# Performance work log

Hardware: AMD Instinct MI355X
Metric: run time of the kernel (lower is better)

Reference implementation:

```python
import jax, jax.numpy as jnp
import numpy as np

B, S, D, H, G = 4, 2048, 1024, 16, 32
HD = D // H
LN_EPS = 1e-5


def _lin_init(key, fan_in, fan_out):
    kw, kb = jax.random.split(key)
    bound = 1.0 / np.sqrt(fan_in)
    W = jax.random.uniform(kw, (fan_in, fan_out), jnp.float32, -bound, bound)
    b = jax.random.uniform(kb, (fan_out,), jnp.float32, -bound, bound)
    return W, b


def setup_inputs() -> dict:
    key = jax.random.key(0)
    ks = jax.random.split(key, 9)
    x = jax.random.normal(ks[0], (B, S, D), jnp.float32)
    geo_features = jax.random.normal(ks[1], (B, G), jnp.float32)
    Wq, bq = _lin_init(ks[2], D, D)
    Wk, bk = _lin_init(ks[3], D, D)
    Wv, bv = _lin_init(ks[4], D, D)
    Wo, bo = _lin_init(ks[5], D, D)
    ge_W1, ge_b1 = _lin_init(ks[6], G, D)
    ln_g = jnp.ones((D,), jnp.float32)
    ln_b = jnp.zeros((D,), jnp.float32)
    ge_W2, ge_b2 = _lin_init(ks[7], D, D)
    gm_W, gm_b = _lin_init(ks[8], D, H)
    return dict(x=x, geo_features=geo_features, Wq=Wq, bq=bq, Wk=Wk, bk=bk,
                Wv=Wv, bv=bv, Wo=Wo, bo=bo, ge_W1=ge_W1, ge_b1=ge_b1,
                ln_g=ln_g, ln_b=ln_b, ge_W2=ge_W2, ge_b2=ge_b2,
                gm_W=gm_W, gm_b=gm_b)


def reference(x, geo_features, Wq, bq, Wk, bk, Wv, bv, Wo, bo,
              ge_W1, ge_b1, ln_g, ln_b, ge_W2, ge_b2, gm_W, gm_b):
    # QKV projections -> (B, H, S, HD)
    def split_heads(t):
        return t.reshape(B, S, H, HD).transpose(0, 2, 1, 3)
    Q = split_heads(x @ Wq + bq)
    K = split_heads(x @ Wk + bk)
    V = split_heads(x @ Wv + bv)

    # geo encoder: Linear -> LayerNorm -> ReLU -> Linear
    h = geo_features @ ge_W1 + ge_b1                      # (B, D)
    mu = jnp.mean(h, axis=-1, keepdims=True)
    var = jnp.mean(jnp.square(h - mu), axis=-1, keepdims=True)
    h = (h - mu) / jnp.sqrt(var + LN_EPS) * ln_g + ln_b
    h = jax.nn.relu(h)
    geo_encoded = h @ ge_W2 + ge_b2                       # (B, D)
    geo_mod = jax.nn.sigmoid(geo_encoded @ gm_W + gm_b)   # (B, H)

    scale = 1.0 / np.sqrt(HD)
    scores = jnp.einsum('bhqd,bhkd->bhqk', Q, K) * scale  # (B, H, S, S)
    scores = scores * (1.0 + geo_mod[:, :, None, None])
    attn = jax.nn.softmax(scores, axis=-1)                # dropout in eval mode: identity
    ctx = jnp.einsum('bhqk,bhkd->bhqd', attn, V)          # (B, H, S, HD)
    ctx = ctx.transpose(0, 2, 1, 3).reshape(B, S, D)
    out = ctx @ Wo + bo
    return out, attn
```

## Files before the change

### kernel.cpp

```cpp
#include <hip/hip_runtime.h>

typedef __attribute__((ext_vector_type(8))) short bf16x8;
typedef __attribute__((ext_vector_type(4))) float f32x4;
typedef __attribute__((ext_vector_type(4))) unsigned short us4;
typedef unsigned short u16;

#define MB (1024*1024)

#define WAITV(N) asm volatile("s_waitcnt vmcnt(" #N ")" ::: "memory")
#define WAITL0() asm volatile("s_waitcnt lgkmcnt(0)" ::: "memory")
#define BAR()    __builtin_amdgcn_s_barrier()
#define SCHEDB() __builtin_amdgcn_sched_barrier(0)

__device__ __forceinline__ u16 f2bf(float f) {
    unsigned u = __float_as_uint(f);
    unsigned r = (u + 0x7fffu + ((u >> 16) & 1u)) >> 16;
    return (u16)r;
}

__device__ __forceinline__ unsigned cvtpk(float a, float b) {
    unsigned r;
    asm("v_cvt_pk_bf16_f32 %0, %1, %2" : "=v"(r) : "v"(a), "v"(b));
    return r;
}

__device__ __forceinline__ f32x4 mfma16(bf16x8 a, bf16x8 b, f32x4 c) {
    return __builtin_amdgcn_mfma_f32_16x16x32_bf16(a, b, c, 0, 0, 0);
}

__device__ __forceinline__ void gload16(const void* g, void* l) {
    __builtin_amdgcn_global_load_lds(
        (__attribute__((address_space(1))) void*)(unsigned long long)g,
        (__attribute__((address_space(3))) void*)l, 16, 0, 0);
}

__global__ __launch_bounds__(256) void k_cvtx(const float* __restrict__ x, u16* __restrict__ xb) {
    const long long i = (long long)blockIdx.x * 256 + threadIdx.x;
    const float4* xp = (const float4*)x;
    float4 a = xp[i*2], b = xp[i*2+1];
    bf16x8 o;
    o[0]=(short)f2bf(a.x); o[1]=(short)f2bf(a.y); o[2]=(short)f2bf(a.z); o[3]=(short)f2bf(a.w);
    o[4]=(short)f2bf(b.x); o[5]=(short)f2bf(b.y); o[6]=(short)f2bf(b.z); o[7]=(short)f2bf(b.w);
    *(bf16x8*)&xb[i*8] = o;
}

__global__ __launch_bounds__(256) void k_wtcvt(const float* __restrict__ W0, const float* __restrict__ W1,
                                               const float* __restrict__ W2, const float* __restrict__ W3,
                                               u16* __restrict__ wt) {
    __shared__ float tl[32][33];
    const int t = threadIdx.x, z = blockIdx.z;
    const float* W = (z==0)?W0:(z==1)?W1:(z==2)?W2:W3;
    const int k0 = blockIdx.x*32, n0 = blockIdx.y*32;
    const int r = t >> 3, c4 = (t & 7) * 4;
    float4 v = *(const float4*)&W[(long long)(k0+r)*1024 + n0 + c4];
    tl[r][c4] = v.x; tl[r][c4+1] = v.y; tl[r][c4+2] = v.z; tl[r][c4+3] = v.w;
    __syncthreads();
    us4 ov;
    ov[0] = f2bf(tl[c4+0][r]); ov[1] = f2bf(tl[c4+1][r]);
    ov[2] = f2bf(tl[c4+2][r]); ov[3] = f2bf(tl[c4+3][r]);
    *(us4*)&wt[((long long)z << 20) + (long long)(n0+r)*1024 + k0 + c4] = ov;
}

__global__ __launch_bounds__(1024) void k_geo(const float* __restrict__ geo, const float* __restrict__ W1,
                                              const float* __restrict__ b1, const float* __restrict__ lng,
                                              const float* __restrict__ lnb, const float* __restrict__ W2,
                                              const float* __restrict__ b2, const float* __restrict__ gmW,
                                              const float* __restrict__ gmb, float* __restrict__ qs) {
    const int b = blockIdx.x, j = threadIdx.x;
    __shared__ float hs[1024];
    __shared__ float ges[1024];
    __shared__ float parts[64][16];
    __shared__ float r1[16], r2[16];
    __shared__ float mu_s, rv_s;

    float acc = b1[j];
    #pragma unroll 8
    for (int g = 0; g < 32; ++g) acc += geo[b*32+g] * W1[(long long)g*1024 + j];
    float s1 = acc, s2 = acc*acc;
    #pragma unroll
    for (int m = 1; m < 64; m <<= 1) { s1 += __shfl_xor(s1, m); s2 += __shfl_xor(s2, m); }
    const int wid = j >> 6, lid = j & 63;
    if (lid == 0) { r1[wid] = s1; r2[wid] = s2; }
    __syncthreads();
    if (j == 0) {
        float S1 = 0.f, S2 = 0.f;
        for (int i = 0; i < 16; ++i) { S1 += r1[i]; S2 += r2[i]; }
        float mu = S1 / 1024.f;
        float var = S2 / 1024.f - mu*mu;
        mu_s = mu; rv_s = rsqrtf(var + 1e-5f);
    }
    __syncthreads();
    float hv = (acc - mu_s) * rv_s * lng[j] + lnb[j];
    hs[j] = fmaxf(hv, 0.f);
    __syncthreads();

    float acc2 = b2[j];
    #pragma unroll 8
    for (int d = 0; d < 1024; ++d) acc2 += hs[d] * W2[(long long)d*1024 + j];
    ges[j] = acc2;
    __syncthreads();

    const int hh = j & 15, seg = j >> 4;
    float part = 0.f;
    #pragma unroll
    for (int dd = 0; dd < 16; ++dd) {
        const int d = seg*16 + dd;
        part += ges[d] * gmW[d*16 + hh];
    }
    parts[seg][hh] = part;
    __syncthreads();
    if (j < 16) {
        float s = gmb[j];
        for (int k = 0; k < 64; ++k) s += parts[k][j];
        qs[b*16 + j] = 0.125f * (1.f + 1.f/(1.f + __expf(-s)));
    }
}

__global__ __launch_bounds__(256) void k_qkv_gemm(const u16* __restrict__ xb, const u16* __restrict__ wtq,
                                                  const float* __restrict__ bq, const float* __restrict__ bk,
                                                  const float* __restrict__ bv, u16* __restrict__ outq) {
    __shared__ u16 lA[128*64];
    __shared__ u16 lB[128*64];
    const int t = threadIdx.x, z = blockIdx.z;
    const int m0 = blockIdx.y * 128, n0 = blockIdx.x * 128;
    const u16* wt = wtq + (long long)z * (1024*1024);
    const float* bias = (z==0) ? bq : (z==1) ? bk : bv;
    u16* out = outq + (long long)z * 8388608;
    const int w = t >> 6, l = t & 63, lm = l & 15, lg = l >> 4;
    const int wr = (w >> 1) * 64, wc = (w & 1) * 64;
    f32x4 acc[4][4] = {};
    const char* gA = (const char*)xb + (long long)(m0 + (t>>3))*2048 + (t&7)*16;
    const char* gB = (const char*)wt + (long long)(n0 + (t>>3))*2048 + (t&7)*16;
    char* lAp = (char*)lA + t*16;
    char* lBp = (char*)lB + t*16;
    for (int k0 = 0; k0 < 1024; k0 += 64) {
        #pragma unroll
        for (int i = 0; i < 4; ++i) {
            gload16(gA + (long long)i*32*2048, lAp + i*4096);
            gload16(gB + (long long)i*32*2048, lBp + i*4096);
        }
        gA += 128; gB += 128;
        __syncthreads();
        #pragma unroll
        for (int kk = 0; kk < 2; ++kk) {
            bf16x8 af[4], bfr[4];
            #pragma unroll
            for (int mi = 0; mi < 4; ++mi)
                af[mi] = *(const bf16x8*)((const char*)lA + (wr + mi*16 + lm)*128 + kk*64 + lg*16);
            #pragma unroll
            for (int ni = 0; ni < 4; ++ni)
                bfr[ni] = *(const bf16x8*)((const char*)lB + (wc + ni*16 + lm)*128 + kk*64 + lg*16);
            #pragma unroll
            for (int mi = 0; mi < 4; ++mi)
                #pragma unroll
                for (int ni = 0; ni < 4; ++ni)
                    acc[mi][ni] = mfma16(bfr[ni], af[mi], acc[mi][ni]);
        }
        __syncthreads();
    }
    #pragma unroll
    for (int mi = 0; mi < 4; ++mi) {
        const int m = m0 + wr + mi*16 + lm;
        const int b = m >> 11, s = m & 2047;
        #pragma unroll
        for (int ni = 0; ni < 4; ++ni) {
            const int nb = n0 + wc + ni*16 + lg*4;
            const float4 bn4 = *(const float4*)&bias[nb];
            const int hh = nb >> 6, d = nb & 63;
            uint2 pk;
            pk.x = cvtpk(acc[mi][ni][0] + bn4.x, acc[mi][ni][1] + bn4.y);
            pk.y = cvtpk(acc[mi][ni][2] + bn4.z, acc[mi][ni][3] + bn4.w);
            *(uint2*)&out[(((long long)b*16 + hh)*2048 + s)*64 + d] = pk;
        }
    }
}

__global__ __launch_bounds__(256) void k_vtrans(const u16* __restrict__ vb, u16* __restrict__ vt) {
    __shared__ u16 tl[64][40];
    const int t = threadIdx.x;
    const int bh = blockIdx.z, s0 = blockIdx.y*64, d0 = blockIdx.x*32;
    const u16* vsrc = vb + (long long)bh*2048*64;
    {
        const int sl = t >> 2, dg = t & 3;
        bf16x8 v = *(const bf16x8*)&vsrc[(long long)(s0+sl)*64 + d0 + dg*8];
        *(bf16x8*)&tl[sl][dg*8] = v;
    }
    __syncthreads();
    {
        const int dl = t >> 3, sg = t & 7;
        bf16x8 o;
        #pragma unroll
        for (int j = 0; j < 8; ++j) o[j] = (short)tl[sg*8+j][dl];
        *(bf16x8*)&vt[((long long)bh*64 + d0+dl)*2048 + s0 + sg*8] = o;
    }
}

__global__ __launch_bounds__(512, 4) void k_attn_ctx(const u16* __restrict__ Qb, const u16* __restrict__ Kb,
                                                     const u16* __restrict__ Vt, const float* __restrict__ qsv,
                                                     float* __restrict__ invg, u16* __restrict__ ctxb) {
    __shared__ char lds[81920];

    const int nl = blockIdx.x;
    const int ob = (nl & 7)*64 + (nl >> 3);
    const int bh = ob >> 3, qt = ob & 7;
    const int t = threadIdx.x, w = t >> 6, l = t & 63, lm = l & 15, lg = l >> 4;
    const int q0 = qt * 256;
    const float qs = qsv[bh];

    const char* KB = (const char*)Kb + (long long)bh * 262144;
    const char* VB = (const char*)Vt + (long long)bh * 262144;

    bf16x8 qf[2][2];
    {
        const char* QB = (const char*)Qb + (long long)bh * 262144;
        #pragma unroll
        for (int ms = 0; ms < 2; ++ms)
            #pragma unroll
            for (int kc = 0; kc < 2; ++kc)
                qf[ms][kc] = *(const bf16x8*)(QB + (long long)(q0 + w*32 + ms*16 + lm)*128 + kc*64 + lg*16);
    }

    const int off = t*16;
    const int row = off >> 7, cbyt = off & 127;
    const int offA = off;
    const int srcK = row*128  + (cbyt ^ ((row & 7) << 4));
    const int srcV = row*4096 + (cbyt ^ ((row & 7) << 4));

    char* lP = lds + 49152;
    float lsum[2] = {0.f, 0.f};
    f32x4 cacc[2][4] = {};

    gload16(KB + srcK, lds + offA);
    gload16(VB + srcV, lds + 24576 + offA);
    gload16(KB + 8192 + srcK, lds + 8192 + offA);
    gload16(VB + 128 + srcV, lds + 24576 + 8192 + offA);
    SCHEDB();
    WAITV(2); BAR(); SCHEDB();

    int cb_ = 0, sb_ = 2;
    for (int kt = 0; kt < 32; ++kt) {
        const int ktn = (kt < 30) ? kt + 2 : 31;
        gload16(KB + (long long)ktn*8192 + srcK, lds + sb_*8192 + offA);
        gload16(VB + (long long)ktn*128 + srcV, lds + 24576 + sb_*8192 + offA);
        SCHEDB();

        const char* kb = lds + cb_*8192;
        #pragma unroll
        for (int ns = 0; ns < 4; ++ns) {
            const int rowb = ns*16 + lm;
            const int tag = (rowb & 7) << 4;
            bf16x8 kf0 = *(const bf16x8*)(kb + rowb*128 + ((lg*16) ^ tag));
            bf16x8 kf1 = *(const bf16x8*)(kb + rowb*128 + ((64 + lg*16) ^ tag));
            #pragma unroll
            for (int ms = 0; ms < 2; ++ms) {
                f32x4 a = {};
                a = mfma16(kf0, qf[ms][0], a);
                a = mfma16(kf1, qf[ms][1], a);
                const float p0 = __expf(a[0]*qs);
                const float p1 = __expf(a[1]*qs);
                const float p2 = __expf(a[2]*qs);
                const float p3 = __expf(a[3]*qs);
                lsum[ms] += (p0 + p1) + (p2 + p3);
                const int prow = w*32 + ms*16 + lm;
                const int ptag = (prow & 7) << 4;
                uint2 pk; pk.x = cvtpk(p0, p1); pk.y = cvtpk(p2, p3);
                *(uint2*)(lP + prow*128 + ((32*ns + 8*lg) ^ ptag)) = pk;
            }
        }
        WAITL0(); SCHEDB();

        const char* vb = lds + 24576 + cb_*8192;
        #pragma unroll
        for (int ks = 0; ks < 2; ++ks) {
            bf16x8 pa[2];
            #pragma unroll
            for (int ms = 0; ms < 2; ++ms) {
                const int prow = w*32 + ms*16 + lm;
                pa[ms] = *(const bf16x8*)(lP + prow*128 + ((ks*64 + lg*16) ^ ((prow & 7) << 4)));
            }
            #pragma unroll
            for (int dn = 0; dn < 4; ++dn) {
                const int rv = dn*16 + lm;
                bf16x8 vf = *(const bf16x8*)(vb + rv*128 + ((ks*64 + lg*16) ^ ((rv & 7) << 4)));
                cacc[0][dn] = mfma16(pa[0], vf, cacc[0][dn]);
                cacc[1][dn] = mfma16(pa[1], vf, cacc[1][dn]);
            }
        }
        WAITV(2); BAR(); SCHEDB();
        cb_ = (cb_ == 2) ? 0 : cb_ + 1;
        sb_ = (sb_ == 2) ? 0 : sb_ + 1;
    }

    float invl[2];
    #pragma unroll
    for (int ms = 0; ms < 2; ++ms) {
        float v = lsum[ms];
        v += __shfl_xor(v, 16);
        v += __shfl_xor(v, 32);
        invl[ms] = 1.f / v;
    }
    if (lg == 0) {
        invg[bh*2048 + q0 + w*32 + lm]      = invl[0];
        invg[bh*2048 + q0 + w*32 + 16 + lm] = invl[1];
    }
    float* fs = (float*)(lP + w*4096);
    if (lg == 0) { fs[lm] = invl[0]; fs[16 + lm] = invl[1]; }
    WAITL0(); SCHEDB();
    f32x4 iv[2];
    iv[0] = *(const f32x4*)&fs[lg*4];
    iv[1] = *(const f32x4*)&fs[16 + lg*4];

    const int b = bh >> 4, hh = bh & 15;
    #pragma unroll
    for (int ms = 0; ms < 2; ++ms)
        #pragma unroll
        for (int dn = 0; dn < 4; ++dn)
            #pragma unroll
            for (int r = 0; r < 4; ++r) {
                const int q = q0 + w*32 + ms*16 + lg*4 + r;
                ctxb[(((long long)b*2048 + q)*16 + hh)*64 + dn*16 + lm] = f2bf(cacc[ms][dn][r] * iv[ms][r]);
            }
}

__global__ __launch_bounds__(256, 4) void k_pwrite(const u16* __restrict__ Qb, const u16* __restrict__ Kb,
                                                   const float* __restrict__ qsv, const float* __restrict__ invg,
                                                   float* __restrict__ attn_out) {
    __shared__ char lds[40960];

    const int nl = blockIdx.x;
    const int ob = (nl & 7)*128 + (nl >> 3);
    const int bh = ob >> 4, qt = ob & 15;
    const int t = threadIdx.x, w = t >> 6, l = t & 63, lm = l & 15, lg = l >> 4;
    const int q0 = qt * 128;
    const float qs = qsv[bh];

    const char* KB = (const char*)Kb + (long long)bh * 262144;

    bf16x8 qf[2][2];
    {
        const char* QB = (const char*)Qb + (long long)bh * 262144;
        #pragma unroll
        for (int ms = 0; ms < 2; ++ms)
            #pragma unroll
            for (int kc = 0; kc < 2; ++kc)
                qf[ms][kc] = *(const bf16x8*)(QB + (long long)(q0 + w*32 + ms*16 + lm)*128 + kc*64 + lg*16);
    }
    float invq[2];
    invq[0] = invg[bh*2048 + q0 + w*32 + lm];
    invq[1] = invg[bh*2048 + q0 + w*32 + 16 + lm];

    int offA[2], srcK[2];
    #pragma unroll
    for (int i = 0; i < 2; ++i) {
        const int off = i*4096 + t*16;
        const int row = off >> 7, cbyt = off & 127;
        offA[i] = off;
        srcK[i] = row*128 + (cbyt ^ ((row & 7) << 4));
    }

    float* aL = attn_out + ((long long)bh*2048 + q0 + w*32 + lm)*2048 + lg*4;

    #pragma unroll
    for (int tt = 0; tt < 4; ++tt)
        #pragma unroll
        for (int i = 0; i < 2; ++i)
            gload16(KB + (long long)tt*8192 + srcK[i], lds + tt*8192 + offA[i]);
    SCHEDB();
    WAITV(6); BAR(); SCHEDB();

    int cur = 0, nb = 4;
    for (int kt = 0; kt < 32; ++kt) {
        const int ktn = (kt < 28) ? kt + 4 : 31;
        #pragma unroll
        for (int i = 0; i < 2; ++i)
            gload16(KB + (long long)ktn*8192 + srcK[i], lds + nb*8192 + offA[i]);
        SCHEDB();

        const char* kb = lds + cur*8192;
        #pragma unroll
        for (int ns = 0; ns < 4; ++ns) {
            const int rowb = ns*16 + lm;
            const int tag = (rowb & 7) << 4;
            bf16x8 kf0 = *(const bf16x8*)(kb + rowb*128 + ((lg*16) ^ tag));
            bf16x8 kf1 = *(const bf16x8*)(kb + rowb*128 + ((64 + lg*16) ^ tag));
            #pragma unroll
            for (int ms = 0; ms < 2; ++ms) {
                f32x4 a = {};
                a = mfma16(kf0, qf[ms][0], a);
                a = mfma16(kf1, qf[ms][1], a);
                f32x4 pv4;
                pv4[0] = __expf(a[0]*qs) * invq[ms];
                pv4[1] = __expf(a[1]*qs) * invq[ms];
                pv4[2] = __expf(a[2]*qs) * invq[ms];
                pv4[3] = __expf(a[3]*qs) * invq[ms];
                *(f32x4*)(aL + ms*32768 + kt*64 + ns*16) = pv4;
            }
        }
        if (kt == 0)      { WAITV(14); }
        else if (kt == 1) { WAITV(22); }
        else if (kt == 2) { WAITV(30); }
        else              { WAITV(38); }
        BAR(); SCHEDB();
        cur = (cur == 4) ? 0 : cur + 1;
        nb  = (nb  == 4) ? 0 : nb  + 1;
    }
}

__global__ __launch_bounds__(256) void k_o_gemm(const u16* __restrict__ ab, const u16* __restrict__ wt,
                                                const float* __restrict__ bo, float* __restrict__ outf) {
    __shared__ u16 lA[128*64];
    __shared__ u16 lB[128*64];
    const int t = threadIdx.x;
    const int m0 = blockIdx.y * 128, n0 = blockIdx.x * 128;
    const int w = t >> 6, l = t & 63, lm = l & 15, lg = l >> 4;
    const int wr = (w >> 1) * 64, wc = (w & 1) * 64;
    f32x4 acc[4][4] = {};
    const char* gA = (const char*)ab + (long long)(m0 + (t>>3))*2048 + (t&7)*16;
    const char* gB = (const char*)wt + (long long)(n0 + (t>>3))*2048 + (t&7)*16;
    char* lAp = (char*)lA + t*16;
    char* lBp = (char*)lB + t*16;
    for (int k0 = 0; k0 < 1024; k0 += 64) {
        #pragma unroll
        for (int i = 0; i < 4; ++i) {
            gload16(gA + (long long)i*32*2048, lAp + i*4096);
            gload16(gB + (long long)i*32*2048, lBp + i*4096);
        }
        gA += 128; gB += 128;
        __syncthreads();
        #pragma unroll
        for (int kk = 0; kk < 2; ++kk) {
            bf16x8 af[4], bfr[4];
            #pragma unroll
            for (int mi = 0; mi < 4; ++mi)
                af[mi] = *(const bf16x8*)((const char*)lA + (wr + mi*16 + lm)*128 + kk*64 + lg*16);
            #pragma unroll
            for (int ni = 0; ni < 4; ++ni)
                bfr[ni] = *(const bf16x8*)((const char*)lB + (wc + ni*16 + lm)*128 + kk*64 + lg*16);
            #pragma unroll
            for (int mi = 0; mi < 4; ++mi)
                #pragma unroll
                for (int ni = 0; ni < 4; ++ni)
                    acc[mi][ni] = mfma16(bfr[ni], af[mi], acc[mi][ni]);
        }
        __syncthreads();
    }
    #pragma unroll
    for (int mi = 0; mi < 4; ++mi) {
        const int m = m0 + wr + mi*16 + lm;
        #pragma unroll
        for (int ni = 0; ni < 4; ++ni) {
            const int nb = n0 + wc + ni*16 + lg*4;
            const float4 bn4 = *(const float4*)&bo[nb];
            f32x4 v = acc[mi][ni];
            v[0] += bn4.x; v[1] += bn4.y; v[2] += bn4.z; v[3] += bn4.w;
            *(f32x4*)&outf[(long long)m*1024 + nb] = v;
        }
    }
}

extern "C" void kernel_launch(void* const* d_in, const int* in_sizes, int n_in,
                              void* d_out, int out_size, void* d_ws, size_t ws_size,
                              hipStream_t stream) {
    const float* x    = (const float*)d_in[0];
    const float* geo  = (const float*)d_in[1];
    const float* Wq   = (const float*)d_in[2];
    const float* bq   = (const float*)d_in[3];
    const float* Wk   = (const float*)d_in[4];
    const float* bk   = (const float*)d_in[5];
    const float* Wv   = (const float*)d_in[6];
    const float* bv   = (const float*)d_in[7];
    const float* Wo   = (const float*)d_in[8];
    const float* bo   = (const float*)d_in[9];
    const float* geW1 = (const float*)d_in[10];
    const float* geb1 = (const float*)d_in[11];
    const float* lng  = (const float*)d_in[12];
    const float* lnb  = (const float*)d_in[13];
    const float* geW2 = (const float*)d_in[14];
    const float* geb2 = (const float*)d_in[15];
    const float* gmW  = (const float*)d_in[16];
    const float* gmb  = (const float*)d_in[17];

    char* ws = (char*)d_ws;
    u16* xb   = (u16*)(ws + 0);
    u16* wt   = (u16*)(ws + 16*(size_t)MB);
    u16* qkv  = (u16*)(ws + 24*(size_t)MB);
    u16* Qb   = qkv;
    u16* Kb   = (u16*)(ws + 40*(size_t)MB);
    u16* Vb   = (u16*)(ws + 56*(size_t)MB);
    u16* Vt   = (u16*)(ws + 72*(size_t)MB);
    u16* ctx  = Vb;
    float* qsb= (float*)(ws + 88*(size_t)MB);
    float* invg = (float*)(ws + 0);

    float* outf = (float*)d_out;
    float* attn = outf + 8388608;

    hipLaunchKernelGGL(k_cvtx,     dim3(4096),      dim3(256),  0, stream, x, xb);
    hipLaunchKernelGGL(k_wtcvt,    dim3(32,32,4),   dim3(256),  0, stream, Wq, Wk, Wv, Wo, wt);
    hipLaunchKernelGGL(k_geo,      dim3(4),         dim3(1024), 0, stream, geo, geW1, geb1, lng, lnb, geW2, geb2, gmW, gmb, qsb);
    hipLaunchKernelGGL(k_qkv_gemm, dim3(8,64,3),    dim3(256),  0, stream, xb, wt, bq, bk, bv, qkv);
    hipLaunchKernelGGL(k_vtrans,   dim3(2,32,64),   dim3(256),  0, stream, Vb, Vt);
    hipLaunchKernelGGL(k_attn_ctx, dim3(512),       dim3(512),  0, stream, Qb, Kb, Vt, qsb, invg, ctx);
    hipLaunchKernelGGL(k_pwrite,   dim3(1024),      dim3(256),  0, stream, Qb, Kb, qsb, invg, attn);
    hipLaunchKernelGGL(k_o_gemm,   dim3(8,64),      dim3(256),  0, stream, ctx, wt + 3*1048576, bo, outf);
}
```

Baseline: 613.3 us.

## Stage attention-probability writes through LDS and split geo encoder across blocks

The probability-write kernel now handles 32 query rows per block, with 4096 blocks instead of 1024. Each wave computes a 16-query by 32-key slice and stages the exp results in a swizzled LDS buffer. Every four key tiles the block writes full 1KB row segments to global memory, giving wide contiguous stores instead of scattered 64-byte pieces. It uses a 3-deep K prefetch ring and lowers the occupancy hint to 2 blocks. Separately, the geo encoder's 1024x1024 matvec, which ran on only 4 blocks, is split into three kernels, one of them spread over 64 blocks, to remove a serial latency hotspot. The cost is extra launches and LDS barriers.

```diff
diff --git a/kernel.cpp b/kernel.cpp
--- a/kernel.cpp
+++ b/kernel.cpp
@@ -61,24 +61,18 @@
     *(us4*)&wt[((long long)z << 20) + (long long)(n0+r)*1024 + k0 + c4] = ov;
 }
 
-__global__ __launch_bounds__(1024) void k_geo(const float* __restrict__ geo, const float* __restrict__ W1,
-                                              const float* __restrict__ b1, const float* __restrict__ lng,
-                                              const float* __restrict__ lnb, const float* __restrict__ W2,
-                                              const float* __restrict__ b2, const float* __restrict__ gmW,
-                                              const float* __restrict__ gmb, float* __restrict__ qs) {
+__global__ __launch_bounds__(1024) void k_geo1(const float* __restrict__ geo, const float* __restrict__ W1,
+                                               const float* __restrict__ b1, const float* __restrict__ lng,
+                                               const float* __restrict__ lnb, float* __restrict__ hr) {
     const int b = blockIdx.x, j = threadIdx.x;
-    __shared__ float hs[1024];
-    __shared__ float ges[1024];
-    __shared__ float parts[64][16];
-    __shared__ float r1[16], r2[16];
-    __shared__ float mu_s, rv_s;
-
     float acc = b1[j];
     #pragma unroll 8
     for (int g = 0; g < 32; ++g) acc += geo[b*32+g] * W1[(long long)g*1024 + j];
     float s1 = acc, s2 = acc*acc;
     #pragma unroll
     for (int m = 1; m < 64; m <<= 1) { s1 += __shfl_xor(s1, m); s2 += __shfl_xor(s2, m); }
+    __shared__ float r1[16], r2[16];
+    __shared__ float mu_s, rv_s;
     const int wid = j >> 6, lid = j & 63;
     if (lid == 0) { r1[wid] = s1; r2[wid] = s2; }
     __syncthreads();
@@ -91,28 +85,51 @@
     }
     __syncthreads();
     float hv = (acc - mu_s) * rv_s * lng[j] + lnb[j];
-    hs[j] = fmaxf(hv, 0.f);
-    __syncthreads();
-
-    float acc2 = b2[j];
-    #pragma unroll 8
-    for (int d = 0; d < 1024; ++d) acc2 += hs[d] * W2[(long long)d*1024 + j];
-    ges[j] = acc2;
-    __syncthreads();
-
-    const int hh = j & 15, seg = j >> 4;
+    hr[b*1024 + j] = fmaxf(hv, 0.f);
+}
+
+__global__ __launch_bounds__(256) void k_geo2(const float* __restrict__ hr, const float* __restrict__ W2,
+                                              const float* __restrict__ b2, float* __restrict__ ge) {
+    const int b = blockIdx.x >> 4, jc = blockIdx.x & 15;
+    const int t = threadIdx.x;
+    __shared__ float hs[1024];
+    __shared__ float parts[4][64];
+    #pragma unroll
+    for (int i = 0; i < 4; ++i) hs[t*4 + i] = hr[b*1024 + t*4 + i];
+    __syncthreads();
+    const int j = jc*64 + (t & 63), dq = t >> 6;
+    float acc = 0.f;
+    #pragma unroll 16
+    for (int dd = 0; dd < 256; ++dd) {
+        const int d = dq*256 + dd;
+        acc += hs[d] * W2[(long long)d*1024 + j];
+    }
+    parts[dq][t & 63] = acc;
+    __syncthreads();
+    if (t < 64) {
+        const int jj = jc*64 + t;
+        ge[b*1024 + jj] = b2[jj] + parts[0][t] + parts[1][t] + parts[2][t] + parts[3][t];
+    }
+}
+
+__global__ __launch_bounds__(1024) void k_geo3(const float* __restrict__ ge, const float* __restrict__ gmW,
+                                               const float* __restrict__ gmb, float* __restrict__ qs) {
+    const int t = threadIdx.x;
+    const int hh = t & 15, b = (t >> 4) & 3, dq = t >> 6;
+    __shared__ float parts[16][64];
     float part = 0.f;
-    #pragma unroll
-    for (int dd = 0; dd < 16; ++dd) {
-        const int d = seg*16 + dd;
-        part += ges[d] * gmW[d*16 + hh];
-    }
-    parts[seg][hh] = part;
-    __syncthreads();
-    if (j < 16) {
-        float s = gmb[j];
-        for (int k = 0; k < 64; ++k) s += parts[k][j];
-        qs[b*16 + j] = 0.125f * (1.f + 1.f/(1.f + __expf(-s)));
+    #pragma unroll 16
+    for (int dd = 0; dd < 64; ++dd) {
+        const int d = dq*64 + dd;
+        part += ge[b*1024 + d] * gmW[d*16 + hh];
+    }
+    parts[dq][b*16 + hh] = part;
+    __syncthreads();
+    if (t < 64) {
+        float s = gmb[t & 15];
+        #pragma unroll
+        for (int k = 0; k < 16; ++k) s += parts[k][t];
+        qs[t] = 0.125f * (1.f + 1.f/(1.f + __expf(-s)));
     }
 }
 
@@ -322,32 +339,29 @@
             }
 }
 
-__global__ __launch_bounds__(256, 4) void k_pwrite(const u16* __restrict__ Qb, const u16* __restrict__ Kb,
+__global__ __launch_bounds__(256, 2) void k_pwrite(const u16* __restrict__ Qb, const u16* __restrict__ Kb,
                                                    const float* __restrict__ qsv, const float* __restrict__ invg,
                                                    float* __restrict__ attn_out) {
-    __shared__ char lds[40960];
+    __shared__ char lds[57344];
 
     const int nl = blockIdx.x;
-    const int ob = (nl & 7)*128 + (nl >> 3);
-    const int bh = ob >> 4, qt = ob & 15;
+    const int ob = (nl & 7)*512 + (nl >> 3);
+    const int bh = ob >> 6, qt = ob & 63;
     const int t = threadIdx.x, w = t >> 6, l = t & 63, lm = l & 15, lg = l >> 4;
-    const int q0 = qt * 128;
+    const int q0 = qt * 32;
+    const int qg = w & 1, kq = w >> 1;
     const float qs = qsv[bh];
 
     const char* KB = (const char*)Kb + (long long)bh * 262144;
 
-    bf16x8 qf[2][2];
+    bf16x8 qf[2];
     {
         const char* QB = (const char*)Qb + (long long)bh * 262144;
         #pragma unroll
-        for (int ms = 0; ms < 2; ++ms)
-            #pragma unroll
-            for (int kc = 0; kc < 2; ++kc)
-                qf[ms][kc] = *(const bf16x8*)(QB + (long long)(q0 + w*32 + ms*16 + lm)*128 + kc*64 + lg*16);
-    }
-    float invq[2];
-    invq[0] = invg[bh*2048 + q0 + w*32 + lm];
-    invq[1] = invg[bh*2048 + q0 + w*32 + 16 + lm];
+        for (int kc = 0; kc < 2; ++kc)
+            qf[kc] = *(const bf16x8*)(QB + (long long)(q0 + qg*16 + lm)*128 + kc*64 + lg*16);
+    }
+    const float invq = invg[bh*2048 + q0 + qg*16 + lm];
 
     int offA[2], srcK[2];
     #pragma unroll
@@ -358,51 +372,62 @@
         srcK[i] = row*128 + (cbyt ^ ((row & 7) << 4));
     }
 
-    float* aL = attn_out + ((long long)bh*2048 + q0 + w*32 + lm)*2048 + lg*4;
-
-    #pragma unroll
-    for (int tt = 0; tt < 4; ++tt)
+    char* lP = lds + 24576;
+
+    #pragma unroll
+    for (int tt = 0; tt < 2; ++tt)
         #pragma unroll
         for (int i = 0; i < 2; ++i)
             gload16(KB + (long long)tt*8192 + srcK[i], lds + tt*8192 + offA[i]);
     SCHEDB();
-    WAITV(6); BAR(); SCHEDB();
-
-    int cur = 0, nb = 4;
+    WAITV(2); BAR(); SCHEDB();
+
     for (int kt = 0; kt < 32; ++kt) {
-        const int ktn = (kt < 28) ? kt + 4 : 31;
-        #pragma unroll
-        for (int i = 0; i < 2; ++i)
-            gload16(KB + (long long)ktn*8192 + srcK[i], lds + nb*8192 + offA[i]);
+        const int ktn = (kt < 30) ? kt + 2 : 31;
+        {
+            char* dst = lds + ((kt + 2) % 3)*8192;
+            #pragma unroll
+            for (int i = 0; i < 2; ++i)
+                gload16(KB + (long long)ktn*8192 + srcK[i], dst + offA[i]);
+        }
         SCHEDB();
 
-        const char* kb = lds + cur*8192;
-        #pragma unroll
-        for (int ns = 0; ns < 4; ++ns) {
-            const int rowb = ns*16 + lm;
-            const int tag = (rowb & 7) << 4;
+        const char* kb = lds + (kt % 3)*8192;
+        #pragma unroll
+        for (int ns = 0; ns < 2; ++ns) {
+            const int rowb = kq*32 + ns*16 + lm;
+            const int tag = (lm & 7) << 4;
             bf16x8 kf0 = *(const bf16x8*)(kb + rowb*128 + ((lg*16) ^ tag));
             bf16x8 kf1 = *(const bf16x8*)(kb + rowb*128 + ((64 + lg*16) ^ tag));
-            #pragma unroll
-            for (int ms = 0; ms < 2; ++ms) {
-                f32x4 a = {};
-                a = mfma16(kf0, qf[ms][0], a);
-                a = mfma16(kf1, qf[ms][1], a);
-                f32x4 pv4;
-                pv4[0] = __expf(a[0]*qs) * invq[ms];
-                pv4[1] = __expf(a[1]*qs) * invq[ms];
-                pv4[2] = __expf(a[2]*qs) * invq[ms];
-                pv4[3] = __expf(a[3]*qs) * invq[ms];
-                *(f32x4*)(aL + ms*32768 + kt*64 + ns*16) = pv4;
+            f32x4 a = {};
+            a = mfma16(kf0, qf[0], a);
+            a = mfma16(kf1, qf[1], a);
+            f32x4 pv4;
+            pv4[0] = __expf(a[0]*qs) * invq;
+            pv4[1] = __expf(a[1]*qs) * invq;
+            pv4[2] = __expf(a[2]*qs) * invq;
+            pv4[3] = __expf(a[3]*qs) * invq;
+            const int prow = qg*16 + lm;
+            const int kwb = ((kt & 3) << 8) + (kq << 7) + (ns << 6) + (lg << 4);
+            *(f32x4*)(lP + prow*1024 + (kwb ^ (lm << 4))) = pv4;
+        }
+
+        if ((kt & 3) == 3) {
+            const int win = kt >> 2;
+            WAITL0(); BAR(); SCHEDB();
+            const int r0 = w*8;
+            #pragma unroll
+            for (int r = 0; r < 8; ++r) {
+                const int rr = r0 + r;
+                f32x4 v = *(const f32x4*)(lP + rr*1024 + ((l*16) ^ ((rr & 15) << 4)));
+                *(f32x4*)(attn_out + ((long long)(bh*2048 + q0 + rr))*2048 + win*256 + l*4) = v;
             }
-        }
-        if (kt == 0)      { WAITV(14); }
-        else if (kt == 1) { WAITV(22); }
-        else if (kt == 2) { WAITV(30); }
-        else              { WAITV(38); }
+            BAR(); SCHEDB();
+        }
+
+        if (((kt & 3) == 3) || (((kt & 3) == 0) && kt > 0)) { WAITV(10); }
+        else                                                { WAITV(2);  }
         BAR(); SCHEDB();
-        cur = (cur == 4) ? 0 : cur + 1;
-        nb  = (nb  == 4) ? 0 : nb  + 1;
     }
 }
 
@@ -490,6 +515,8 @@
     u16* Vt   = (u16*)(ws + 72*(size_t)MB);
     u16* ctx  = Vb;
     float* qsb= (float*)(ws + 88*(size_t)MB);
+    float* hr = (float*)(ws + 88*(size_t)MB + 4096);
+    float* ge = (float*)(ws + 88*(size_t)MB + 65536);
     float* invg = (float*)(ws + 0);
 
     float* outf = (float*)d_out;
@@ -497,10 +524,12 @@
 
     hipLaunchKernelGGL(k_cvtx,     dim3(4096),      dim3(256),  0, stream, x, xb);
     hipLaunchKernelGGL(k_wtcvt,    dim3(32,32,4),   dim3(256),  0, stream, Wq, Wk, Wv, Wo, wt);
-    hipLaunchKernelGGL(k_geo,      dim3(4),         dim3(1024), 0, stream, geo, geW1, geb1, lng, lnb, geW2, geb2, gmW, gmb, qsb);
+    hipLaunchKernelGGL(k_geo1,     dim3(4),         dim3(1024), 0, stream, geo, geW1, geb1, lng, lnb, hr);
+    hipLaunchKernelGGL(k_geo2,     dim3(64),        dim3(256),  0, stream, hr, geW2, geb2, ge);
+    hipLaunchKernelGGL(k_geo3,     dim3(1),         dim3(1024), 0, stream, ge, gmW, gmb, qsb);
     hipLaunchKernelGGL(k_qkv_gemm, dim3(8,64,3),    dim3(256),  0, stream, xb, wt, bq, bk, bv, qkv);
     hipLaunchKernelGGL(k_vtrans,   dim3(2,32,64),   dim3(256),  0, stream, Vb, Vt);
     hipLaunchKernelGGL(k_attn_ctx, dim3(512),       dim3(512),  0, stream, Qb, Kb, Vt, qsb, invg, ctx);
-    hipLaunchKernelGGL(k_pwrite,   dim3(1024),      dim3(256),  0, stream, Qb, Kb, qsb, invg, attn);
+    hipLaunchKernelGGL(k_pwrite,   dim3(4096),      dim3(256),  0, stream, Qb, Kb, qsb, invg, attn);
     hipLaunchKernelGGL(k_o_gemm,   dim3(8,64),      dim3(256),  0, stream, ctx, wt + 3*1048576, bo, outf);
 }
```

New measurement: 554.2 us. 1.11x faster.
